# Optimization experiments

Hardware: AMD Instinct MI355X
Metric: run time of the kernel (lower is better)

Reference implementation:

```python
import jax, jax.numpy as jnp
import numpy as np

DIM = 256
NUM_HEADS = 8
HEAD_DIM = DIM // NUM_HEADS


def setup_inputs() -> dict:
    key = jax.random.key(0)
    k_x, k_wq, k_bq, k_wp, k_bp = jax.random.split(key, 5)
    B, C, H, W = 2, DIM, 48, 48
    x = jax.random.normal(k_x, (B, C, H, W), dtype=jnp.float32)
    # 1x1 convs are pointwise matmuls: store weights as [out, in]
    w_qkv = jax.random.normal(k_wq, (3 * C, C), dtype=jnp.float32) * (1.0 / np.sqrt(C))
    b_qkv = jax.random.normal(k_bq, (3 * C,), dtype=jnp.float32) * 0.01
    w_proj = jax.random.normal(k_wp, (C, C), dtype=jnp.float32) * (1.0 / np.sqrt(C))
    b_proj = jax.random.normal(k_bp, (C,), dtype=jnp.float32) * 0.01
    return {"x": x, "w_qkv": w_qkv, "b_qkv": b_qkv, "w_proj": w_proj, "b_proj": b_proj}


def reference(x, w_qkv, b_qkv, w_proj, b_proj):
    B, C, H, W = x.shape
    N = H * W
    # qkv 1x1 conv -> pointwise channel matmul
    qkv = jnp.einsum('bchw,oc->bohw', x, w_qkv) + b_qkv[None, :, None, None]
    q, k, v = jnp.split(qkv, 3, axis=1)  # each [B, C, H, W]
    q = q.reshape(B, NUM_HEADS, HEAD_DIM, N)
    k = k.reshape(B, NUM_HEADS, HEAD_DIM, N)
    v = v.reshape(B, NUM_HEADS, HEAD_DIM, N)
    scale = 1.0 / (HEAD_DIM ** 0.5)
    attn = jnp.einsum('bhdn,bhdm->bhnm', q, k) * scale  # [B, H, N, N]
    attn = jax.nn.softmax(attn, axis=-1)
    out = jnp.einsum('bhnm,bhdm->bhdn', attn, v)  # [B, heads, head_dim, N]
    out = out.reshape(B, C, H, W)
    out = jnp.einsum('bchw,oc->bohw', out, w_proj) + b_proj[None, :, None, None]
    return out + x
```

## Files before the change

### kernel.cpp

```cpp
#include <hip/hip_runtime.h>
#include <math.h>

#define C_DIM 256
#define NH 8
#define HD 32
#define BATCH 2
#define NPIX 2304
#define TK 64
#define NGRP (NPIX / 16)
#define TPB 18

typedef __attribute__((ext_vector_type(8))) short bf16x8;
typedef __attribute__((ext_vector_type(4))) float f32x4;

#define OFF_XT  0u
#define OFF_Q   1179648u
#define OFF_K   2359296u
#define OFF_V   3538944u
#define OFF_OT  4718592u
#define OFF_WQ  5898240u
#define OFF_WP  6094848u
#define OFF_F32 6160384u

__device__ __forceinline__ unsigned short f2b(float f) {
    union { float f; unsigned int u; } c; c.f = f;
    unsigned int u = c.u + 0x7FFFu + ((c.u >> 16) & 1u);
    return (unsigned short)(u >> 16);
}
__device__ __forceinline__ unsigned int pk2(float lo, float hi) {
    union { float f; unsigned int u; } a, b;
    a.f = lo; b.f = hi;
    return __builtin_amdgcn_perm(b.u + 0x8000u, a.u + 0x8000u, 0x07060302u);
}
__device__ __forceinline__ unsigned int cvtpk(float lo, float hi) {
    unsigned int r;
    asm("v_cvt_pk_bf16_f32 %0, %1, %2" : "=v"(r) : "v"(lo), "v"(hi));
    return r;
}
__device__ __forceinline__ float fexp2(float x) {
#if __has_builtin(__builtin_amdgcn_exp2f)
    return __builtin_amdgcn_exp2f(x);
#else
    return exp2f(x);
#endif
}

__global__ __launch_bounds__(256) void prep_xt(
        const float* __restrict__ x, unsigned short* __restrict__ xT)
{
    __shared__ unsigned short t_s[64][72];
    const int tid = threadIdx.x;
    const int n0 = blockIdx.x * 64, c0 = blockIdx.y * 64, b = blockIdx.z;
    const int nl = tid & 63, cq = tid >> 6;
    #pragma unroll
    for (int p = 0; p < 8; ++p) {
        const int c = p * 8 + cq * 2;
        const float f0 = x[((size_t)b * C_DIM + c0 + c) * NPIX + n0 + nl];
        const float f1 = x[((size_t)b * C_DIM + c0 + c + 1) * NPIX + n0 + nl];
        *(unsigned int*)&t_s[nl][c] = pk2(f0, f1);
    }
    __syncthreads();
    const int row = tid >> 2, jq = tid & 3;
    #pragma unroll
    for (int hh = 0; hh < 2; ++hh) {
        const int jl = jq * 2 + hh;
        const int jg = blockIdx.y * 8 + jl;
        const int ngrp = blockIdx.x * 4 + (row >> 4);
        unsigned short* dst = xT + (((size_t)b * NGRP + ngrp) * 32 + jg) * 128 + (row & 15) * 8;
        *(uint4*)dst = *(uint4*)&t_s[row][jl * 8];
    }
}

__global__ __launch_bounds__(256) void prep_w(
        const float* __restrict__ wqkv, const float* __restrict__ wproj,
        unsigned short* __restrict__ wq, unsigned short* __restrict__ wp)
{
    const int t = blockIdx.x * 256 + threadIdx.x;
    const float* src; unsigned short* dst;
    if (t < 24576) {
        const int m = t >> 5, j = t & 31;
        src = wqkv + ((size_t)m * C_DIM + j * 8);
        dst = wq + ((size_t)((m >> 4) * 32 + j) * 16 + (m & 15)) * 8;
    } else {
        const int t2 = t - 24576, m = t2 >> 5, j = t2 & 31;
        src = wproj + ((size_t)m * C_DIM + j * 8);
        dst = wp + ((size_t)((m >> 4) * 32 + j) * 16 + (m & 15)) * 8;
    }
    const float4 f0 = *(const float4*)src, f1 = *(const float4*)(src + 4);
    *(uint4*)dst = make_uint4(pk2(f0.x, f0.y), pk2(f0.z, f0.w),
                              pk2(f1.x, f1.y), pk2(f1.z, f1.w));
}

__global__ __launch_bounds__(256, 2) void qkv_gemm(
        const unsigned short* __restrict__ xT, const unsigned short* __restrict__ wq,
        const float* __restrict__ bias,
        unsigned short* __restrict__ Qg, unsigned short* __restrict__ Kg,
        unsigned short* __restrict__ Vg)
{
    __shared__ unsigned short eplds[4][2560];
    const int tid = threadIdx.x, wv = tid >> 6, lane = tid & 63;
    const int l15 = lane & 15, quad = lane >> 4;
    const int n0 = blockIdx.x * 256, my = blockIdx.y, b = blockIdx.z;
    const int nw = n0 + wv * 64;

    bf16x8 af[2][8];
    #pragma unroll
    for (int mt = 0; mt < 2; ++mt)
        #pragma unroll
        for (int kc = 0; kc < 8; ++kc)
            af[mt][kc] = *(const bf16x8*)(wq +
                ((size_t)((my * 2 + mt) * 32 + kc * 4 + quad) * 16 + l15) * 8);

    f32x4 acc[2][4];
    #pragma unroll
    for (int mt = 0; mt < 2; ++mt)
        #pragma unroll
        for (int s = 0; s < 4; ++s) acc[mt][s] = (f32x4){0.f, 0.f, 0.f, 0.f};

    #pragma unroll
    for (int sub = 0; sub < 4; ++sub) {
        const int ngrp = (nw + sub * 16) >> 4;
        const unsigned short* bp = xT + ((size_t)b * NGRP + ngrp) * 32 * 128;
        #pragma unroll
        for (int kc = 0; kc < 8; ++kc) {
            const bf16x8 bf = *(const bf16x8*)(bp + (size_t)(kc * 4 + quad) * 128 + l15 * 8);
            acc[0][sub] = __builtin_amdgcn_mfma_f32_16x16x32_bf16(af[0][kc], bf, acc[0][sub], 0, 0, 0);
            acc[1][sub] = __builtin_amdgcn_mfma_f32_16x16x32_bf16(af[1][kc], bf, acc[1][sub], 0, 0, 0);
        }
    }

    const int which = my >> 3;
    const int h = my & 7, bh = b * NH + h;
    float4 b4[2];
    b4[0] = *(const float4*)(bias + my * 32 + quad * 4);
    b4[1] = *(const float4*)(bias + my * 32 + 16 + quad * 4);
    unsigned short* wl = eplds[wv];

    if (which < 2) {
        const float sc = (which == 0) ? 0.2550348576f : 1.0f;
        #pragma unroll
        for (int mt = 0; mt < 2; ++mt)
            #pragma unroll
            for (int sub = 0; sub < 4; ++sub) {
                const float v0 = (acc[mt][sub][0] + b4[mt].x) * sc;
                const float v1 = (acc[mt][sub][1] + b4[mt].y) * sc;
                const float v2 = (acc[mt][sub][2] + b4[mt].z) * sc;
                const float v3 = (acc[mt][sub][3] + b4[mt].w) * sc;
                *(uint2*)&wl[(sub * 16 + l15) * 40 + mt * 16 + quad * 4] =
                    make_uint2(pk2(v0, v1), pk2(v2, v3));
            }
        unsigned short* dst = ((which == 0) ? Qg : Kg)
                            + ((size_t)bh * NPIX + nw + lane) * HD;
        #pragma unroll
        for (int i = 0; i < 4; ++i)
            *((uint4*)dst + i) = *(uint4*)&wl[lane * 40 + i * 8];
    } else {
        #pragma unroll
        for (int mt = 0; mt < 2; ++mt)
            #pragma unroll
            for (int sub = 0; sub < 4; ++sub) {
                wl[(mt * 16 + quad * 4 + 0) * 72 + sub * 16 + l15] = f2b(acc[mt][sub][0] + b4[mt].x);
                wl[(mt * 16 + quad * 4 + 1) * 72 + sub * 16 + l15] = f2b(acc[mt][sub][1] + b4[mt].y);
                wl[(mt * 16 + quad * 4 + 2) * 72 + sub * 16 + l15] = f2b(acc[mt][sub][2] + b4[mt].z);
                wl[(mt * 16 + quad * 4 + 3) * 72 + sub * 16 + l15] = f2b(acc[mt][sub][3] + b4[mt].w);
            }
        const int row = lane >> 1, seg = (lane & 1) * 32;
        unsigned short* dst = Vg + ((size_t)bh * HD + row) * NPIX + nw + seg;
        #pragma unroll
        for (int i = 0; i < 4; ++i)
            *((uint4*)dst + i) = *(uint4*)&wl[row * 72 + seg + i * 8];
    }
}

__global__ __launch_bounds__(256, 4) void attn_kernel(
        const unsigned short* __restrict__ Qg, const unsigned short* __restrict__ Kg,
        const unsigned short* __restrict__ Vg,
        float* __restrict__ OtP, float* __restrict__ lsumP)
{
    __shared__ unsigned short k_s[2][TK][40];
    __shared__ unsigned short v_s[2][HD][76];
    __shared__ unsigned short p_s[4][16][76];

    const int tid  = threadIdx.x;
    const int wv   = tid >> 6;
    const int lane = tid & 63;
    const int l15  = lane & 15;
    const int quad = lane >> 4;
    const int bh   = blockIdx.x;
    const int q0   = blockIdx.y * 64;
    const int sp   = blockIdx.z;
    const int t0   = sp * TPB;

    const unsigned short* Qh = Qg + (size_t)bh * NPIX * HD;
    const unsigned short* Kh = Kg + (size_t)bh * NPIX * HD;
    const unsigned short* Vh = Vg + (size_t)bh * HD * NPIX;

    const bf16x8 q_frag = *(const bf16x8*)(Qh + (size_t)(q0 + wv * 16 + l15) * HD + quad * 8);
    const bf16x8 onesf = {16256, 16256, 16256, 16256, 16256, 16256, 16256, 16256};

    const int kr = tid >> 2, kc = (tid & 3) * 8;
    const int vd = tid >> 3, vc = (tid & 7) * 8;

    uint4 kreg = *(const uint4*)(Kh + (size_t)(t0 * TK + kr) * HD + kc);
    uint4 vreg = *(const uint4*)(Vh + (size_t)vd * NPIX + t0 * TK + vc);
    *(uint4*)&k_s[0][kr][kc] = kreg;
    *(uint4*)&v_s[0][vd][vc] = vreg;

    f32x4 o0 = {0.f, 0.f, 0.f, 0.f};
    f32x4 o1 = {0.f, 0.f, 0.f, 0.f};
    f32x4 ol = {0.f, 0.f, 0.f, 0.f};

    for (int t = 0; t < TPB; ++t) {
        const int cur = t & 1;
        if (t + 1 < TPB) {
            const int k0 = (t0 + t + 1) * TK;
            kreg = *(const uint4*)(Kh + (size_t)(k0 + kr) * HD + kc);
            vreg = *(const uint4*)(Vh + (size_t)vd * NPIX + k0 + vc);
        }
        __syncthreads();

        f32x4 s[4];
        #pragma unroll
        for (int kg = 0; kg < 4; ++kg) {
            const bf16x8 kf = *(const bf16x8*)&k_s[cur][kg * 16 + l15][quad * 8];
            s[kg] = __builtin_amdgcn_mfma_f32_16x16x32_bf16(kf, q_frag,
                        (f32x4){0.f, 0.f, 0.f, 0.f}, 0, 0, 0);
        }

        #pragma unroll
        for (int kg = 0; kg < 4; ++kg) {
            const float p0 = fexp2(s[kg][0]);
            const float p1 = fexp2(s[kg][1]);
            const float p2 = fexp2(s[kg][2]);
            const float p3 = fexp2(s[kg][3]);
            *(uint2*)&p_s[wv][l15][kg * 16 + quad * 4] =
                make_uint2(cvtpk(p0, p1), cvtpk(p2, p3));
        }

        #pragma unroll
        for (int kc2 = 0; kc2 < 2; ++kc2) {
            const bf16x8 pf  = *(const bf16x8*)&p_s[wv][l15][kc2 * 32 + quad * 8];
            const bf16x8 vf0 = *(const bf16x8*)&v_s[cur][l15][kc2 * 32 + quad * 8];
            const bf16x8 vf1 = *(const bf16x8*)&v_s[cur][16 + l15][kc2 * 32 + quad * 8];
            o0 = __builtin_amdgcn_mfma_f32_16x16x32_bf16(vf0, pf, o0, 0, 0, 0);
            o1 = __builtin_amdgcn_mfma_f32_16x16x32_bf16(vf1, pf, o1, 0, 0, 0);
            ol = __builtin_amdgcn_mfma_f32_16x16x32_bf16(onesf, pf, ol, 0, 0, 0);
        }

        if (t + 1 < TPB) {
            *(uint4*)&k_s[cur ^ 1][kr][kc] = kreg;
            *(uint4*)&v_s[cur ^ 1][vd][vc] = vreg;
        }
    }

    __syncthreads();
    float* pp = (float*)&p_s[wv][0][0];
    #pragma unroll
    for (int r = 0; r < 4; ++r) {
        pp[l15 * 36 + quad * 4 + r]      = o0[r];
        pp[l15 * 36 + 16 + quad * 4 + r] = o1[r];
    }
    if (quad == 0)
        lsumP[((size_t)sp * 16 + bh) * NPIX + q0 + wv * 16 + l15] = ol[0];
    __syncthreads();
    const int q = lane >> 2, off = (lane & 3) * 8;
    float* dst = OtP + (((size_t)sp * 16 + bh) * NPIX + q0 + wv * 16 + q) * 32 + off;
    *(float4*)dst       = *(float4*)&pp[q * 36 + off];
    *((float4*)dst + 1) = *(float4*)&pp[q * 36 + off + 4];
}

__global__ __launch_bounds__(256) void norm_kernel(
        const float* __restrict__ OtP, const float* __restrict__ lsumP,
        unsigned short* __restrict__ OtT)
{
    const int t = blockIdx.x * 256 + threadIdx.x;
    const int q = t >> 2, jq = t & 3;
    const int bh = blockIdx.y;
    const float* pa = OtP + ((size_t)bh * NPIX + q) * 32 + jq * 8;
    const float* pb = OtP + ((size_t)(16 + bh) * NPIX + q) * 32 + jq * 8;
    const float inv = 1.f / (lsumP[(size_t)bh * NPIX + q] +
                             lsumP[(size_t)(16 + bh) * NPIX + q]);
    const int b = bh >> 3, h = bh & 7;
    unsigned short* cell = OtT + (((size_t)b * NGRP + (q >> 4)) * 32 + h * 4) * 128
                         + (q & 15) * 8 + jq * 128;
    const float4 a0 = *(const float4*)(pa);
    const float4 a1 = *(const float4*)(pa + 4);
    const float4 b0 = *(const float4*)(pb);
    const float4 b1 = *(const float4*)(pb + 4);
    const float o0 = (a0.x + b0.x) * inv, o1 = (a0.y + b0.y) * inv;
    const float o2 = (a0.z + b0.z) * inv, o3 = (a0.w + b0.w) * inv;
    const float o4 = (a1.x + b1.x) * inv, o5 = (a1.y + b1.y) * inv;
    const float o6 = (a1.z + b1.z) * inv, o7 = (a1.w + b1.w) * inv;
    *(uint4*)cell = make_uint4(cvtpk(o0, o1), cvtpk(o2, o3),
                               cvtpk(o4, o5), cvtpk(o6, o7));
}

__global__ __launch_bounds__(256) void proj_gemm(
        const unsigned short* __restrict__ OtT, const unsigned short* __restrict__ wp,
        const float* __restrict__ bias, const float* __restrict__ x,
        float* __restrict__ out)
{
    __shared__ float plds[4][576];
    const int tid = threadIdx.x, wv = tid >> 6, lane = tid & 63;
    const int l15 = lane & 15, quad = lane >> 4;
    const int n0 = blockIdx.x * 128, my = blockIdx.y, b = blockIdx.z;
    const int nw = n0 + wv * 32;

    bf16x8 af[8];
    #pragma unroll
    for (int kc = 0; kc < 8; ++kc)
        af[kc] = *(const bf16x8*)(wp + ((size_t)(my * 32 + kc * 4 + quad) * 16 + l15) * 8);

    f32x4 acc[2];
    acc[0] = (f32x4){0.f, 0.f, 0.f, 0.f};
    acc[1] = (f32x4){0.f, 0.f, 0.f, 0.f};

    #pragma unroll
    for (int sub = 0; sub < 2; ++sub) {
        const int ngrp = (nw + sub * 16) >> 4;
        const unsigned short* bp = OtT + ((size_t)b * NGRP + ngrp) * 32 * 128;
        #pragma unroll
        for (int kc = 0; kc < 8; ++kc) {
            const bf16x8 bf = *(const bf16x8*)(bp + (size_t)(kc * 4 + quad) * 128 + l15 * 8);
            acc[sub] = __builtin_amdgcn_mfma_f32_16x16x32_bf16(af[kc], bf, acc[sub], 0, 0, 0);
        }
    }

    float* wl = plds[wv];
    #pragma unroll
    for (int sub = 0; sub < 2; ++sub) {
        wl[(quad * 4 + 0) * 36 + sub * 16 + l15] = acc[sub][0];
        wl[(quad * 4 + 1) * 36 + sub * 16 + l15] = acc[sub][1];
        wl[(quad * 4 + 2) * 36 + sub * 16 + l15] = acc[sub][2];
        wl[(quad * 4 + 3) * 36 + sub * 16 + l15] = acc[sub][3];
    }
    const int m0 = my * 16;
    #pragma unroll
    for (int p = 0; p < 2; ++p) {
        const int row = p * 8 + (lane >> 3), cn = (lane & 7) * 4;
        const int c = m0 + row;
        const size_t idx = ((size_t)b * C_DIM + c) * NPIX + nw + cn;
        const f32x4 v = *(const f32x4*)&wl[row * 36 + cn];
        const f32x4 r = *(const f32x4*)(x + idx);
        const float bv = bias[c];
        f32x4 o;
        o[0] = v[0] + bv + r[0]; o[1] = v[1] + bv + r[1];
        o[2] = v[2] + bv + r[2]; o[3] = v[3] + bv + r[3];
        *(f32x4*)(out + idx) = o;
    }
}

extern "C" void kernel_launch(void* const* d_in, const int* in_sizes, int n_in,
                              void* d_out, int out_size, void* d_ws, size_t ws_size,
                              hipStream_t stream)
{
    const float* x      = (const float*)d_in[0];
    const float* w_qkv  = (const float*)d_in[1];
    const float* b_qkv  = (const float*)d_in[2];
    const float* w_proj = (const float*)d_in[3];
    const float* b_proj = (const float*)d_in[4];
    float* out = (float*)d_out;

    unsigned short* ws = (unsigned short*)d_ws;
    unsigned short* xT  = ws + OFF_XT;
    unsigned short* Qg  = ws + OFF_Q;
    unsigned short* Kg  = ws + OFF_K;
    unsigned short* Vg  = ws + OFF_V;
    unsigned short* OtT = ws + OFF_OT;
    unsigned short* wq  = ws + OFF_WQ;
    unsigned short* wp  = ws + OFF_WP;
    float* fws   = (float*)(ws + OFF_F32);
    float* OtP   = fws;
    float* lsumP = fws + 4718592;

    prep_xt<<<dim3(36, 4, 2), 256, 0, stream>>>(x, xT);
    prep_w<<<dim3(128), 256, 0, stream>>>(w_qkv, w_proj, wq, wp);
    qkv_gemm<<<dim3(9, 24, 2), 256, 0, stream>>>(xT, wq, b_qkv, Qg, Kg, Vg);
    attn_kernel<<<dim3(16, 36, 2), 256, 0, stream>>>(Qg, Kg, Vg, OtP, lsumP);
    norm_kernel<<<dim3(36, 16), 256, 0, stream>>>(OtP, lsumP, OtT);
    proj_gemm<<<dim3(18, 16, 2), 256, 0, stream>>>(OtT, wp, b_proj, x, out);
}
```

Measured before the change: 114.7 us.

## Keep softmax P in registers via permuted K layout; merge prep kernels

The K tile rows are permuted when written to shared memory so that the score MFMA output fragments line up with the B-operand layout of the PV MFMA. The exponentiated probabilities are then packed straight into bf16x8 registers, which removes the per-tile LDS round trip through p_s. The epilogue gets its own per-wave buffer and drops two block barriers. The two prep kernels are also merged into one launch. The risks are a wrong row permutation producing incorrect results, and a larger LDS footprint reducing occupancy.

```diff
diff --git a/kernel.cpp b/kernel.cpp
--- a/kernel.cpp
+++ b/kernel.cpp
@@ -45,50 +45,51 @@
 #endif
 }
 
-__global__ __launch_bounds__(256) void prep_xt(
-        const float* __restrict__ x, unsigned short* __restrict__ xT)
-{
-    __shared__ unsigned short t_s[64][72];
-    const int tid = threadIdx.x;
-    const int n0 = blockIdx.x * 64, c0 = blockIdx.y * 64, b = blockIdx.z;
-    const int nl = tid & 63, cq = tid >> 6;
-    #pragma unroll
-    for (int p = 0; p < 8; ++p) {
-        const int c = p * 8 + cq * 2;
-        const float f0 = x[((size_t)b * C_DIM + c0 + c) * NPIX + n0 + nl];
-        const float f1 = x[((size_t)b * C_DIM + c0 + c + 1) * NPIX + n0 + nl];
-        *(unsigned int*)&t_s[nl][c] = pk2(f0, f1);
-    }
-    __syncthreads();
-    const int row = tid >> 2, jq = tid & 3;
-    #pragma unroll
-    for (int hh = 0; hh < 2; ++hh) {
-        const int jl = jq * 2 + hh;
-        const int jg = blockIdx.y * 8 + jl;
-        const int ngrp = blockIdx.x * 4 + (row >> 4);
-        unsigned short* dst = xT + (((size_t)b * NGRP + ngrp) * 32 + jg) * 128 + (row & 15) * 8;
-        *(uint4*)dst = *(uint4*)&t_s[row][jl * 8];
-    }
-}
-
-__global__ __launch_bounds__(256) void prep_w(
+__global__ __launch_bounds__(256) void prep_all(
+        const float* __restrict__ x, unsigned short* __restrict__ xT,
         const float* __restrict__ wqkv, const float* __restrict__ wproj,
         unsigned short* __restrict__ wq, unsigned short* __restrict__ wp)
 {
-    const int t = blockIdx.x * 256 + threadIdx.x;
-    const float* src; unsigned short* dst;
-    if (t < 24576) {
-        const int m = t >> 5, j = t & 31;
-        src = wqkv + ((size_t)m * C_DIM + j * 8);
-        dst = wq + ((size_t)((m >> 4) * 32 + j) * 16 + (m & 15)) * 8;
+    __shared__ unsigned short t_s[64][72];
+    const int bid = blockIdx.x;
+    const int tid = threadIdx.x;
+    if (bid < 288) {
+        const int bx = bid % 36, by = (bid / 36) & 3, bz = bid / 144;
+        const int n0 = bx * 64, c0 = by * 64, b = bz;
+        const int nl = tid & 63, cq = tid >> 6;
+        #pragma unroll
+        for (int p = 0; p < 8; ++p) {
+            const int c = p * 8 + cq * 2;
+            const float f0 = x[((size_t)b * C_DIM + c0 + c) * NPIX + n0 + nl];
+            const float f1 = x[((size_t)b * C_DIM + c0 + c + 1) * NPIX + n0 + nl];
+            *(unsigned int*)&t_s[nl][c] = pk2(f0, f1);
+        }
+        __syncthreads();
+        const int row = tid >> 2, jq = tid & 3;
+        #pragma unroll
+        for (int hh = 0; hh < 2; ++hh) {
+            const int jl = jq * 2 + hh;
+            const int jg = by * 8 + jl;
+            const int ngrp = bx * 4 + (row >> 4);
+            unsigned short* dst = xT + (((size_t)b * NGRP + ngrp) * 32 + jg) * 128 + (row & 15) * 8;
+            *(uint4*)dst = *(uint4*)&t_s[row][jl * 8];
+        }
     } else {
-        const int t2 = t - 24576, m = t2 >> 5, j = t2 & 31;
-        src = wproj + ((size_t)m * C_DIM + j * 8);
-        dst = wp + ((size_t)((m >> 4) * 32 + j) * 16 + (m & 15)) * 8;
-    }
-    const float4 f0 = *(const float4*)src, f1 = *(const float4*)(src + 4);
-    *(uint4*)dst = make_uint4(pk2(f0.x, f0.y), pk2(f0.z, f0.w),
-                              pk2(f1.x, f1.y), pk2(f1.z, f1.w));
+        const int t = (bid - 288) * 256 + tid;
+        const float* src; unsigned short* dst;
+        if (t < 24576) {
+            const int m = t >> 5, j = t & 31;
+            src = wqkv + ((size_t)m * C_DIM + j * 8);
+            dst = wq + ((size_t)((m >> 4) * 32 + j) * 16 + (m & 15)) * 8;
+        } else {
+            const int t2 = t - 24576, m = t2 >> 5, j = t2 & 31;
+            src = wproj + ((size_t)m * C_DIM + j * 8);
+            dst = wp + ((size_t)((m >> 4) * 32 + j) * 16 + (m & 15)) * 8;
+        }
+        const float4 f0 = *(const float4*)src, f1 = *(const float4*)(src + 4);
+        *(uint4*)dst = make_uint4(pk2(f0.x, f0.y), pk2(f0.z, f0.w),
+                                  pk2(f1.x, f1.y), pk2(f1.z, f1.w));
+    }
 }
 
 __global__ __launch_bounds__(256, 2) void qkv_gemm(
@@ -179,7 +180,7 @@
 {
     __shared__ unsigned short k_s[2][TK][40];
     __shared__ unsigned short v_s[2][HD][76];
-    __shared__ unsigned short p_s[4][16][76];
+    __shared__ float ep_s[4][16][36];
 
     const int tid  = threadIdx.x;
     const int wv   = tid >> 6;
@@ -199,11 +200,12 @@
     const bf16x8 onesf = {16256, 16256, 16256, 16256, 16256, 16256, 16256, 16256};
 
     const int kr = tid >> 2, kc = (tid & 3) * 8;
+    const int ksl = (kr & 0x23) | ((kr & 0x04) << 2) | ((kr & 0x18) >> 1);
     const int vd = tid >> 3, vc = (tid & 7) * 8;
 
     uint4 kreg = *(const uint4*)(Kh + (size_t)(t0 * TK + kr) * HD + kc);
     uint4 vreg = *(const uint4*)(Vh + (size_t)vd * NPIX + t0 * TK + vc);
-    *(uint4*)&k_s[0][kr][kc] = kreg;
+    *(uint4*)&k_s[0][ksl][kc] = kreg;
     *(uint4*)&v_s[0][vd][vc] = vreg;
 
     f32x4 o0 = {0.f, 0.f, 0.f, 0.f};
@@ -227,34 +229,33 @@
                         (f32x4){0.f, 0.f, 0.f, 0.f}, 0, 0, 0);
         }
 
-        #pragma unroll
-        for (int kg = 0; kg < 4; ++kg) {
-            const float p0 = fexp2(s[kg][0]);
-            const float p1 = fexp2(s[kg][1]);
-            const float p2 = fexp2(s[kg][2]);
-            const float p3 = fexp2(s[kg][3]);
-            *(uint2*)&p_s[wv][l15][kg * 16 + quad * 4] =
-                make_uint2(cvtpk(p0, p1), cvtpk(p2, p3));
-        }
-
+        bf16x8 pf[2];
         #pragma unroll
         for (int kc2 = 0; kc2 < 2; ++kc2) {
-            const bf16x8 pf  = *(const bf16x8*)&p_s[wv][l15][kc2 * 32 + quad * 8];
+            union { unsigned int u[4]; bf16x8 v; } c;
+            c.u[0] = cvtpk(fexp2(s[2 * kc2][0]),     fexp2(s[2 * kc2][1]));
+            c.u[1] = cvtpk(fexp2(s[2 * kc2][2]),     fexp2(s[2 * kc2][3]));
+            c.u[2] = cvtpk(fexp2(s[2 * kc2 + 1][0]), fexp2(s[2 * kc2 + 1][1]));
+            c.u[3] = cvtpk(fexp2(s[2 * kc2 + 1][2]), fexp2(s[2 * kc2 + 1][3]));
+            pf[kc2] = c.v;
+        }
+
+        #pragma unroll
+        for (int kc2 = 0; kc2 < 2; ++kc2) {
             const bf16x8 vf0 = *(const bf16x8*)&v_s[cur][l15][kc2 * 32 + quad * 8];
             const bf16x8 vf1 = *(const bf16x8*)&v_s[cur][16 + l15][kc2 * 32 + quad * 8];
-            o0 = __builtin_amdgcn_mfma_f32_16x16x32_bf16(vf0, pf, o0, 0, 0, 0);
-            o1 = __builtin_amdgcn_mfma_f32_16x16x32_bf16(vf1, pf, o1, 0, 0, 0);
-            ol = __builtin_amdgcn_mfma_f32_16x16x32_bf16(onesf, pf, ol, 0, 0, 0);
+            o0 = __builtin_amdgcn_mfma_f32_16x16x32_bf16(vf0, pf[kc2], o0, 0, 0, 0);
+            o1 = __builtin_amdgcn_mfma_f32_16x16x32_bf16(vf1, pf[kc2], o1, 0, 0, 0);
+            ol = __builtin_amdgcn_mfma_f32_16x16x32_bf16(onesf, pf[kc2], ol, 0, 0, 0);
         }
 
         if (t + 1 < TPB) {
-            *(uint4*)&k_s[cur ^ 1][kr][kc] = kreg;
+            *(uint4*)&k_s[cur ^ 1][ksl][kc] = kreg;
             *(uint4*)&v_s[cur ^ 1][vd][vc] = vreg;
         }
     }
 
-    __syncthreads();
-    float* pp = (float*)&p_s[wv][0][0];
+    float* pp = &ep_s[wv][0][0];
     #pragma unroll
     for (int r = 0; r < 4; ++r) {
         pp[l15 * 36 + quad * 4 + r]      = o0[r];
@@ -262,7 +263,6 @@
     }
     if (quad == 0)
         lsumP[((size_t)sp * 16 + bh) * NPIX + q0 + wv * 16 + l15] = ol[0];
-    __syncthreads();
     const int q = lane >> 2, off = (lane & 3) * 8;
     float* dst = OtP + (((size_t)sp * 16 + bh) * NPIX + q0 + wv * 16 + q) * 32 + off;
     *(float4*)dst       = *(float4*)&pp[q * 36 + off];
@@ -373,8 +373,7 @@
     float* OtP   = fws;
     float* lsumP = fws + 4718592;
 
-    prep_xt<<<dim3(36, 4, 2), 256, 0, stream>>>(x, xT);
-    prep_w<<<dim3(128), 256, 0, stream>>>(w_qkv, w_proj, wq, wp);
+    prep_all<<<dim3(416), 256, 0, stream>>>(x, xT, w_qkv, w_proj, wq, wp);
     qkv_gemm<<<dim3(9, 24, 2), 256, 0, stream>>>(xT, wq, b_qkv, Qg, Kg, Vg);
     attn_kernel<<<dim3(16, 36, 2), 256, 0, stream>>>(Qg, Kg, Vg, OtP, lsumP);
     norm_kernel<<<dim3(36, 16), 256, 0, stream>>>(OtP, lsumP, OtT);
```

After: 106.0 us. 7.6% less time.
